# Performance work log

Measured on AMD Instinct MI355X. Metric: run time of the kernel, lower is better.

The kernel has to match this reference:

```python
import jax, jax.numpy as jnp
import numpy as np

EMBED_DIM = 768
NUM_HEADS = 12
HEAD_DIM = EMBED_DIM // NUM_HEADS


def setup_inputs() -> dict:
    key = jax.random.key(0)
    ks = jax.random.split(key, 9)
    B, S, D = 2, 2048, EMBED_DIM
    scale = 1.0 / np.sqrt(D)
    x = jax.random.normal(ks[0], (B, S, D), dtype=jnp.float32)
    Wq = jax.random.normal(ks[1], (D, D), dtype=jnp.float32) * scale
    bq = jax.random.normal(ks[2], (D,), dtype=jnp.float32) * 0.01
    Wk = jax.random.normal(ks[3], (D, D), dtype=jnp.float32) * scale
    bk = jax.random.normal(ks[4], (D,), dtype=jnp.float32) * 0.01
    Wv = jax.random.normal(ks[5], (D, D), dtype=jnp.float32) * scale
    bv = jax.random.normal(ks[6], (D,), dtype=jnp.float32) * 0.01
    Wo = jax.random.normal(ks[7], (D, D), dtype=jnp.float32) * scale
    bo = jax.random.normal(ks[8], (D,), dtype=jnp.float32) * 0.01
    return {"x": x, "Wq": Wq, "bq": bq, "Wk": Wk, "bk": bk,
            "Wv": Wv, "bv": bv, "Wo": Wo, "bo": bo}


def reference(x, Wq, bq, Wk, bk, Wv, bv, Wo, bo):
    B, S, D = x.shape
    H, Dh = NUM_HEADS, HEAD_DIM
    # separate QKV projections (weights stored [in, out] so y = x @ W + b)
    q = (x @ Wq + bq).reshape(B, S, H, Dh)
    k = (x @ Wk + bk).reshape(B, S, H, Dh)
    v = (x @ Wv + bv).reshape(B, S, H, Dh)
    # NOTE: original module applies NO 1/sqrt(head_dim) scaling
    scores = jnp.einsum('bqhd,bkhd->bhqk', q, k)          # [B,H,S,S] materialized
    attn = jax.nn.softmax(scores, axis=-1)
    ctx = jnp.einsum('bhqk,bkhd->bqhd', attn, v)          # [B,S,H,Dh]
    out = ctx.reshape(B, S, D) @ Wo + bo
    return out
```

## Files before the change

kernel.cpp:

```cpp
#include <hip/hip_runtime.h>
#include <hip/hip_bf16.h>


typedef __attribute__((ext_vector_type(8))) short short8;
typedef __attribute__((ext_vector_type(4))) float float4e;
typedef __attribute__((ext_vector_type(16))) float f32x16;

__device__ __forceinline__ ushort f2bf(float f) {
    union { float f; unsigned u; } v; v.f = f;
    unsigned r = v.u + 0x7FFF + ((v.u >> 16) & 1);
    return (ushort)(r >> 16);
}

__device__ __forceinline__ unsigned pk2bf(float a, float b) {
    float2 t; t.x = a; t.y = b;
    __hip_bfloat162 h = __float22bfloat162_rn(t);
    union { __hip_bfloat162 h; unsigned u; } cv; cv.h = h;
    return cv.u;
}

__device__ __forceinline__ void async_cp16(const ushort* g, ushort* l) {
    __builtin_amdgcn_global_load_lds(
        (const __attribute__((address_space(1))) unsigned int*)g,
        (__attribute__((address_space(3))) unsigned int*)l,
        16, 0, 0);
}

__global__ __launch_bounds__(256) void cast_f32_bf16(
    const float* __restrict__ in, ushort* __restrict__ out, int n4)
{
    int i = blockIdx.x * blockDim.x + threadIdx.x;
    if (i < n4) {
        float4 v = *(const float4*)&in[(size_t)i * 4];
        ushort4 o;
        o.x = f2bf(v.x); o.y = f2bf(v.y); o.z = f2bf(v.z); o.w = f2bf(v.w);
        *(ushort4*)&out[(size_t)i * 4] = o;
    }
}

__global__ __launch_bounds__(256) void transpose_cast_w4(
    const float* __restrict__ W0, const float* __restrict__ W1,
    const float* __restrict__ W2, const float* __restrict__ W3,
    ushort* __restrict__ WtBase)
{
    __shared__ float t[64][65];
    const int z = blockIdx.z;
    const float* W = (z == 0) ? W0 : (z == 1) ? W1 : (z == 2) ? W2 : W3;
    ushort* Wt = WtBase + (size_t)z * (768u * 768u);

    const int tid = threadIdx.x;
    const int c  = tid & 63;
    const int rg = tid >> 6;
    const int k0 = blockIdx.y * 64, n0 = blockIdx.x * 64;
    #pragma unroll
    for (int r = 0; r < 16; ++r) {
        const int row = rg * 16 + r;
        t[row][c] = W[(size_t)(k0 + row) * 768 + n0 + c];
    }
    __syncthreads();
    #pragma unroll
    for (int r = 0; r < 16; ++r) {
        const int row = rg * 16 + r;
        Wt[(size_t)(n0 + row) * 768 + k0 + c] = f2bf(t[c][row]);
    }
}

__global__ __launch_bounds__(256) void transpose_v(
    const ushort* __restrict__ Vb, ushort* __restrict__ VT)
{
    __shared__ ushort t[64][72];
    const int tid = threadIdx.x;
    const int b = blockIdx.z, h = blockIdx.y, s0 = blockIdx.x * 64;
    const int lr = tid >> 3;
    const int lc = (tid & 7) * 8;

    #pragma unroll
    for (int half = 0; half < 64; half += 32) {
        const int row = lr + half;
        *(uint4*)&t[row][lc] =
            *(const uint4*)&Vb[(size_t)(b * 2048 + s0 + row) * 768 + h * 64 + lc];
    }
    __syncthreads();
    #pragma unroll
    for (int half = 0; half < 64; half += 32) {
        const int d = lr + half;
        ushort tmp[8];
        #pragma unroll
        for (int i = 0; i < 8; ++i) tmp[i] = t[lc + i][d];
        *(uint4*)&VT[((size_t)(b * 12 + h) * 64 + d) * 2048 + s0 + lc] =
            *(const uint4*)tmp;
    }
}

__global__ __launch_bounds__(256) void gemm_qkv_fused(
    const ushort* __restrict__ A, const ushort* __restrict__ Bt,
    const float* __restrict__ bq, const float* __restrict__ bk,
    const float* __restrict__ bv, ushort* __restrict__ Outbase)
{
    constexpr int K = 768;
    __shared__ ushort As[2][128][32];
    __shared__ ushort Bs[2][128][32];

    const int tid  = threadIdx.x;
    const int w    = tid >> 6;
    const int lane = tid & 63;
    const int l16  = lane & 15;
    const int quad = lane >> 4;
    const int wr   = (w >> 1) * 64;
    const int wc   = (w & 1) * 64;
    const int row0 = blockIdx.y * 128, col0 = blockIdx.x * 128;

    const int r4 = lane >> 2;
    const int c8 = (lane & 3) * 8;

    float4e acc[4][4];
    #pragma unroll
    for (int mi = 0; mi < 4; ++mi)
        #pragma unroll
        for (int ni = 0; ni < 4; ++ni) acc[mi][ni] = (float4e){0.f,0.f,0.f,0.f};

    #pragma unroll
    for (int i = 0; i < 2; ++i) {
        const int rr = w * 32 + i * 16;
        async_cp16(&A [(size_t)(row0 + rr + r4) * K + c8], &As[0][rr][0]);
        async_cp16(&Bt[(size_t)(col0 + rr + r4) * K + c8], &Bs[0][rr][0]);
    }
    __syncthreads();

    for (int k0 = 0; k0 < K; k0 += 32) {
        const int cur = (k0 >> 5) & 1;
        if (k0 + 32 < K) {
            #pragma unroll
            for (int i = 0; i < 2; ++i) {
                const int rr = w * 32 + i * 16;
                async_cp16(&A [(size_t)(row0 + rr + r4) * K + k0 + 32 + c8],
                           &As[cur ^ 1][rr][0]);
                async_cp16(&Bt[(size_t)(col0 + rr + r4) * K + k0 + 32 + c8],
                           &Bs[cur ^ 1][rr][0]);
            }
        }

        short8 af[4], bf[4];
        #pragma unroll
        for (int i = 0; i < 4; ++i) {
            af[i] = *(const short8*)&As[cur][wr + i * 16 + l16][quad * 8];
            bf[i] = *(const short8*)&Bs[cur][wc + i * 16 + l16][quad * 8];
        }
        #pragma unroll
        for (int mi = 0; mi < 4; ++mi)
            #pragma unroll
            for (int ni = 0; ni < 4; ++ni)
                acc[mi][ni] = __builtin_amdgcn_mfma_f32_16x16x32_bf16(
                    af[mi], bf[ni], acc[mi][ni], 0, 0, 0);
        __syncthreads();
    }

    const int seg = (col0 >= 1536) ? 2 : (col0 >= 768 ? 1 : 0);
    const float* bias = (seg == 0) ? bq : (seg == 1) ? bk : bv;
    const int ncol0 = col0 - seg * 768 + wc;
    ushort* outp = Outbase + (size_t)seg * (4096u * 768u);

    #pragma unroll
    for (int ni = 0; ni < 4; ++ni) {
        const int col = ncol0 + ni * 16 + l16;
        const float bs = bias[col];
        #pragma unroll
        for (int mi = 0; mi < 4; ++mi) {
            #pragma unroll
            for (int r = 0; r < 4; ++r) {
                const int row = row0 + wr + mi * 16 + quad * 4 + r;
                outp[(size_t)row * 768 + col] = f2bf(acc[mi][ni][r] + bs);
            }
        }
    }
}

__global__ __launch_bounds__(256) void gemm_wo_128(
    const ushort* __restrict__ A, const ushort* __restrict__ Bt,
    const float* __restrict__ bias, float* __restrict__ Cout)
{
    constexpr int K = 768, N = 768;
    __shared__ ushort As[2][128][32];
    __shared__ ushort Bs[2][128][32];

    const int tid  = threadIdx.x;
    const int w    = tid >> 6;
    const int lane = tid & 63;
    const int l16  = lane & 15;
    const int quad = lane >> 4;
    const int wr   = (w >> 1) * 64;
    const int wc   = (w & 1) * 64;
    const int row0 = blockIdx.y * 128, col0 = blockIdx.x * 128;

    const int r4 = lane >> 2;
    const int c8 = (lane & 3) * 8;

    float4e acc[4][4];
    #pragma unroll
    for (int mi = 0; mi < 4; ++mi)
        #pragma unroll
        for (int ni = 0; ni < 4; ++ni) acc[mi][ni] = (float4e){0.f,0.f,0.f,0.f};

    #pragma unroll
    for (int i = 0; i < 2; ++i) {
        const int rr = w * 32 + i * 16;
        async_cp16(&A [(size_t)(row0 + rr + r4) * K + c8], &As[0][rr][0]);
        async_cp16(&Bt[(size_t)(col0 + rr + r4) * K + c8], &Bs[0][rr][0]);
    }
    __syncthreads();

    for (int k0 = 0; k0 < K; k0 += 32) {
        const int cur = (k0 >> 5) & 1;
        if (k0 + 32 < K) {
            #pragma unroll
            for (int i = 0; i < 2; ++i) {
                const int rr = w * 32 + i * 16;
                async_cp16(&A [(size_t)(row0 + rr + r4) * K + k0 + 32 + c8],
                           &As[cur ^ 1][rr][0]);
                async_cp16(&Bt[(size_t)(col0 + rr + r4) * K + k0 + 32 + c8],
                           &Bs[cur ^ 1][rr][0]);
            }
        }

        short8 af[4], bf[4];
        #pragma unroll
        for (int i = 0; i < 4; ++i) {
            af[i] = *(const short8*)&As[cur][wr + i * 16 + l16][quad * 8];
            bf[i] = *(const short8*)&Bs[cur][wc + i * 16 + l16][quad * 8];
        }
        #pragma unroll
        for (int mi = 0; mi < 4; ++mi)
            #pragma unroll
            for (int ni = 0; ni < 4; ++ni)
                acc[mi][ni] = __builtin_amdgcn_mfma_f32_16x16x32_bf16(
                    af[mi], bf[ni], acc[mi][ni], 0, 0, 0);
        __syncthreads();
    }

    #pragma unroll
    for (int ni = 0; ni < 4; ++ni) {
        const int col = col0 + wc + ni * 16 + l16;
        const float bs = bias[col];
        #pragma unroll
        for (int mi = 0; mi < 4; ++mi) {
            #pragma unroll
            for (int r = 0; r < 4; ++r) {
                const int row = row0 + wr + mi * 16 + quad * 4 + r;
                Cout[(size_t)row * N + col] = acc[mi][ni][r] + bs;
            }
        }
    }
}

__global__ __launch_bounds__(512, 4) void attn_mfma(
    const ushort* __restrict__ Qg, const ushort* __restrict__ Kgl,
    const ushort* __restrict__ VT, ushort* __restrict__ Ctx)
{
    constexpr int S = 2048, D = 768;
    __shared__ union {
        struct {
            ushort Ks [2][128][64];
            ushort Vts[2][64][128];
        } s;
        struct {
            float Osc[6][2048];
            float Msc[6][32];
            float Lsc[6][32];
        } c;
    } U;

    const int tid  = threadIdx.x;
    const int w    = tid >> 6;
    const int qg   = w & 1;
    const int ks   = w >> 1;
    const int lane = tid & 63;
    const int l31  = lane & 31;
    const int hi   = lane >> 5;
    const int b = blockIdx.z, h = blockIdx.y, q0 = blockIdx.x * 64;
    const size_t hc = (size_t)h * 64;

    const size_t qrow = (size_t)(b * S + q0 + qg * 32 + l31) * D + hc + hi * 8;
    short8 yq[4];
    #pragma unroll
    for (int dc = 0; dc < 4; ++dc) yq[dc] = *(const short8*)&Qg[qrow + dc * 16];

    const int sr  = tid >> 3;
    const int kgr = (tid & 7) ^ (sr & 7);
    const ushort* srcK = &Kgl[(size_t)(b * S + sr) * D + hc + kgr * 8];
    const int vr  = tid >> 4;
    const int vgr = (tid & 15) ^ (vr & 7);
    const ushort* srcV = &VT[((size_t)(b * 12 + h) * 64 + vr) * 2048 + vgr * 8];
    ushort* dK0 = &U.s.Ks [0][w * 8][0];
    ushort* dK1 = &U.s.Ks [1][w * 8][0];
    ushort* dV0 = &U.s.Vts[0][w * 4][0];
    ushort* dV1 = &U.s.Vts[1][w * 4][0];

    int okf[4];
    #pragma unroll
    for (int dc = 0; dc < 4; ++dc)
        okf[dc] = (ks * 32 + l31) * 64 + ((dc * 2 + hi) ^ (l31 & 7)) * 8;
    int ovo[2][2][2];
    #pragma unroll
    for (int a = 0; a < 2; ++a)
        #pragma unroll
        for (int m = 0; m < 2; ++m)
            #pragma unroll
            for (int c2 = 0; c2 < 2; ++c2)
                ovo[a][m][c2] = (a * 32 + l31) * 128 +
                    ((ks * 4 + m * 2 + c2) ^ (l31 & 7)) * 8 + hi * 4;

    float m_ = -1e30f, l_ = 0.f;
    f32x16 oa0, oa1;
    #pragma unroll
    for (int i = 0; i < 16; ++i) { oa0[i] = 0.f; oa1[i] = 0.f; }

    async_cp16(srcK,                  dK0);
    async_cp16(srcK + (size_t)64 * D, dK0 + 64 * 64);
    async_cp16(srcV,                  dV0);
    async_cp16(srcV + 32 * 2048,      dV0 + 32 * 128);
    __syncthreads();

    #pragma unroll 2
    for (int t = 0; t < 16; ++t) {
        const int cur = t & 1;
        const ushort* ksb = cur ? &U.s.Ks [1][0][0] : &U.s.Ks [0][0][0];
        const ushort* vsb = cur ? &U.s.Vts[1][0][0] : &U.s.Vts[0][0][0];
        if (t + 1 < 16) {
            const size_t kn = (size_t)(t + 1) * 128;
            ushort* dK = cur ? dK0 : dK1;
            ushort* dV = cur ? dV0 : dV1;
            async_cp16(srcK + kn * D,              dK);
            async_cp16(srcK + (kn + 64) * D,       dK + 64 * 64);
            async_cp16(srcV + kn,                  dV);
            async_cp16(srcV + kn + 32 * 2048,      dV + 32 * 128);
        }

        f32x16 sa;
        #pragma unroll
        for (int i = 0; i < 16; ++i) sa[i] = 0.f;
        __builtin_amdgcn_s_setprio(1);
        #pragma unroll
        for (int dc = 0; dc < 4; ++dc) {
            const short8 xk = *(const short8*)&ksb[okf[dc]];
            sa = __builtin_amdgcn_mfma_f32_32x32x16_bf16(xk, yq[dc], sa, 0, 0, 0);
        }
        __builtin_amdgcn_s_setprio(0);

        float mx = sa[0];
        #pragma unroll
        for (int r = 1; r < 16; ++r) mx = fmaxf(mx, sa[r]);
        mx = fmaxf(mx, __shfl_xor(mx, 32, 64));

        const bool full = !__all(mx - m_ <= 8.f);
        if (full) {
            const float mn = fmaxf(m_, mx);
            const float alpha = __expf(m_ - mn);
            l_ *= alpha;
            m_ = mn;
            #pragma unroll
            for (int i = 0; i < 16; ++i) { oa0[i] *= alpha; oa1[i] *= alpha; }
        }

        float p[16], ps = 0.f;
        #pragma unroll
        for (int r = 0; r < 16; ++r) {
            p[r] = __expf(sa[r] - m_);
            ps += p[r];
        }
        ps += __shfl_xor(ps, 32, 64);
        l_ += ps;

        union { unsigned u[4]; short8 s8; } pa0, pa1;
        pa0.u[0] = pk2bf(p[0],  p[1]);  pa0.u[1] = pk2bf(p[2],  p[3]);
        pa0.u[2] = pk2bf(p[4],  p[5]);  pa0.u[3] = pk2bf(p[6],  p[7]);
        pa1.u[0] = pk2bf(p[8],  p[9]);  pa1.u[1] = pk2bf(p[10], p[11]);
        pa1.u[2] = pk2bf(p[12], p[13]); pa1.u[3] = pk2bf(p[14], p[15]);

        __builtin_amdgcn_s_setprio(1);
        {
            union { uint2 v2[2]; short8 s8; } xv;
            xv.v2[0] = *(const uint2*)&vsb[ovo[0][0][0]];
            xv.v2[1] = *(const uint2*)&vsb[ovo[0][0][1]];
            oa0 = __builtin_amdgcn_mfma_f32_32x32x16_bf16(xv.s8, pa0.s8, oa0, 0, 0, 0);
            xv.v2[0] = *(const uint2*)&vsb[ovo[0][1][0]];
            xv.v2[1] = *(const uint2*)&vsb[ovo[0][1][1]];
            oa0 = __builtin_amdgcn_mfma_f32_32x32x16_bf16(xv.s8, pa1.s8, oa0, 0, 0, 0);
            xv.v2[0] = *(const uint2*)&vsb[ovo[1][0][0]];
            xv.v2[1] = *(const uint2*)&vsb[ovo[1][0][1]];
            oa1 = __builtin_amdgcn_mfma_f32_32x32x16_bf16(xv.s8, pa0.s8, oa1, 0, 0, 0);
            xv.v2[0] = *(const uint2*)&vsb[ovo[1][1][0]];
            xv.v2[1] = *(const uint2*)&vsb[ovo[1][1][1]];
            oa1 = __builtin_amdgcn_mfma_f32_32x32x16_bf16(xv.s8, pa1.s8, oa1, 0, 0, 0);
        }
        __builtin_amdgcn_s_setprio(0);

        __syncthreads();
    }

    if (ks > 0) {
        const int slot = (ks - 1) * 2 + qg;
        float* ob = &U.c.Osc[slot][lane * 32];
        #pragma unroll
        for (int g = 0; g < 4; ++g) {
            float4 v0, v1;
            v0.x = oa0[g * 4 + 0]; v0.y = oa0[g * 4 + 1];
            v0.z = oa0[g * 4 + 2]; v0.w = oa0[g * 4 + 3];
            v1.x = oa1[g * 4 + 0]; v1.y = oa1[g * 4 + 1];
            v1.z = oa1[g * 4 + 2]; v1.w = oa1[g * 4 + 3];
            *(float4*)&ob[(( g     ) ^ (lane & 7)) * 4] = v0;
            *(float4*)&ob[(((g + 4)) ^ (lane & 7)) * 4] = v1;
        }
        if (hi == 0) {
            U.c.Msc[slot][l31] = m_;
            U.c.Lsc[slot][l31] = l_;
        }
    }
    __syncthreads();
    if (ks == 0) {
        const float m1 = U.c.Msc[qg][l31];
        const float m2 = U.c.Msc[2 + qg][l31];
        const float m3 = U.c.Msc[4 + qg][l31];
        const float M  = fmaxf(fmaxf(m_, m1), fmaxf(m2, m3));
        const float a0 = __expf(m_ - M), a1 = __expf(m1 - M),
                    a2 = __expf(m2 - M), a3 = __expf(m3 - M);
        const float l1 = U.c.Lsc[qg][l31];
        const float l2 = U.c.Lsc[2 + qg][l31];
        const float l3 = U.c.Lsc[4 + qg][l31];
        const float inv = 1.0f / (l_ * a0 + l1 * a1 + l2 * a2 + l3 * a3);

        float o[32];
        #pragma unroll
        for (int i = 0; i < 16; ++i) { o[i] = oa0[i] * a0; o[16 + i] = oa1[i] * a0; }
        #pragma unroll
        for (int s = 0; s < 3; ++s) {
            const float as = (s == 0) ? a1 : (s == 1) ? a2 : a3;
            const float* ob = &U.c.Osc[s * 2 + qg][lane * 32];
            #pragma unroll
            for (int gg = 0; gg < 8; ++gg) {
                const float4 v = *(const float4*)&ob[(gg ^ (lane & 7)) * 4];
                o[gg * 4 + 0] += v.x * as;
                o[gg * 4 + 1] += v.y * as;
                o[gg * 4 + 2] += v.z * as;
                o[gg * 4 + 3] += v.w * as;
            }
        }

        const size_t crow = (size_t)(b * S + q0 + qg * 32 + l31) * D + hc;
        #pragma unroll
        for (int a = 0; a < 2; ++a)
            #pragma unroll
            for (int rq = 0; rq < 4; ++rq) {
                const int base = a * 16 + rq * 4;
                uint2 ov;
                ov.x = pk2bf(o[base + 0] * inv, o[base + 1] * inv);
                ov.y = pk2bf(o[base + 2] * inv, o[base + 3] * inv);
                *(uint2*)&Ctx[crow + a * 32 + rq * 8 + hi * 4] = ov;
            }
    }
}

extern "C" void kernel_launch(void* const* d_in, const int* in_sizes, int n_in,
                              void* d_out, int out_size, void* d_ws, size_t ws_size,
                              hipStream_t stream)
{
    const float* x  = (const float*)d_in[0];
    const float* Wq = (const float*)d_in[1];
    const float* bq = (const float*)d_in[2];
    const float* Wk = (const float*)d_in[3];
    const float* bk = (const float*)d_in[4];
    const float* Wv = (const float*)d_in[5];
    const float* bv = (const float*)d_in[6];
    const float* Wo = (const float*)d_in[7];
    const float* bo = (const float*)d_in[8];

    const int M = 4096, D = 768;
    const size_t XE = (size_t)M * D;
    const size_t WE = (size_t)D * D;

    ushort* xb   = (ushort*)d_ws;
    ushort* wtq  = xb   + XE;
    ushort* wto  = wtq  + 3 * WE;
    ushort* qb   = wto  + WE;
    ushort* kb   = qb   + XE;
    ushort* vb   = kb   + XE;
    ushort* ctxb = vb   + XE;
    ushort* vt   = xb;

    cast_f32_bf16<<<(int)(XE / 4 / 256), 256, 0, stream>>>(x, xb, (int)(XE / 4));

    transpose_cast_w4<<<dim3(12, 12, 4), 256, 0, stream>>>(Wq, Wk, Wv, Wo, wtq);

    gemm_qkv_fused<<<dim3(2304 / 128, 4096 / 128), 256, 0, stream>>>(
        xb, wtq, bq, bk, bv, qb);

    transpose_v<<<dim3(32, 12, 2), 256, 0, stream>>>(vb, vt);

    attn_mfma<<<dim3(2048 / 64, 12, 2), 512, 0, stream>>>(qb, kb, vt, ctxb);

    gemm_wo_128<<<dim3(768 / 128, 4096 / 128), 256, 0, stream>>>(
        ctxb, wto, bo, (float*)d_out);
}
```

Before: 182.4 us.

## Load V fragments directly from global in MFMA order, remap blocks by XCD

The V tile is no longer staged through LDS. transpose_v now writes V^T in a permuted column order so that each lane can load its MFMA operand as one 16-byte global load per fragment. This frees LDS, and the launch-bounds occupancy hint is raised from 4 to 6. The attention grid becomes 1D and is remapped so that the blocks on each XCD share the same (batch, head) groups, to improve L2 reuse of K and V. The max reduction is rewritten as a tree. The risk is exposed global-load latency for V inside the loop, since those loads are not prefetched.

After: 257.6 us. 41.3% more time.

```diff
diff --git a/kernel.cpp b/kernel.cpp
--- a/kernel.cpp
+++ b/kernel.cpp
@@ -73,6 +73,8 @@
     const int b = blockIdx.z, h = blockIdx.y, s0 = blockIdx.x * 64;
     const int lr = tid >> 3;
     const int lc = (tid & 7) * 8;
+    const int g  = tid & 7;
+    const int nb = s0 + (g >> 1) * 16 + (g & 1) * 4;
 
     #pragma unroll
     for (int half = 0; half < 64; half += 32) {
@@ -87,8 +89,9 @@
         ushort tmp[8];
         #pragma unroll
         for (int i = 0; i < 8; ++i) tmp[i] = t[lc + i][d];
-        *(uint4*)&VT[((size_t)(b * 12 + h) * 64 + d) * 2048 + s0 + lc] =
-            *(const uint4*)tmp;
+        const size_t row = ((size_t)(b * 12 + h) * 64 + d) * 2048;
+        *(uint2*)&VT[row + nb]     = *(const uint2*)&tmp[0];
+        *(uint2*)&VT[row + nb + 8] = *(const uint2*)&tmp[4];
     }
 }
 
@@ -252,16 +255,13 @@
     }
 }
 
-__global__ __launch_bounds__(512, 4) void attn_mfma(
+__global__ __launch_bounds__(512, 6) void attn_mfma(
     const ushort* __restrict__ Qg, const ushort* __restrict__ Kgl,
     const ushort* __restrict__ VT, ushort* __restrict__ Ctx)
 {
     constexpr int S = 2048, D = 768;
     __shared__ union {
-        struct {
-            ushort Ks [2][128][64];
-            ushort Vts[2][64][128];
-        } s;
+        ushort Ks[2][128][64];
         struct {
             float Osc[6][2048];
             float Msc[6][32];
@@ -276,7 +276,12 @@
     const int lane = tid & 63;
     const int l31  = lane & 31;
     const int hi   = lane >> 5;
-    const int b = blockIdx.z, h = blockIdx.y, q0 = blockIdx.x * 64;
+
+    const int lin = blockIdx.x;
+    const int xcd = lin & 7, sl = lin >> 3;
+    const int grp = xcd * 3 + (sl >> 5);
+    const int q0  = (sl & 31) * 64;
+    const int h   = grp % 12, b = grp / 12;
     const size_t hc = (size_t)h * 64;
 
     const size_t qrow = (size_t)(b * S + q0 + qg * 32 + l31) * D + hc + hi * 8;
@@ -287,27 +292,16 @@
     const int sr  = tid >> 3;
     const int kgr = (tid & 7) ^ (sr & 7);
     const ushort* srcK = &Kgl[(size_t)(b * S + sr) * D + hc + kgr * 8];
-    const int vr  = tid >> 4;
-    const int vgr = (tid & 15) ^ (vr & 7);
-    const ushort* srcV = &VT[((size_t)(b * 12 + h) * 64 + vr) * 2048 + vgr * 8];
-    ushort* dK0 = &U.s.Ks [0][w * 8][0];
-    ushort* dK1 = &U.s.Ks [1][w * 8][0];
-    ushort* dV0 = &U.s.Vts[0][w * 4][0];
-    ushort* dV1 = &U.s.Vts[1][w * 4][0];
+    ushort* dK0 = &U.Ks[0][w * 8][0];
+    ushort* dK1 = &U.Ks[1][w * 8][0];
 
     int okf[4];
     #pragma unroll
     for (int dc = 0; dc < 4; ++dc)
         okf[dc] = (ks * 32 + l31) * 64 + ((dc * 2 + hi) ^ (l31 & 7)) * 8;
-    int ovo[2][2][2];
-    #pragma unroll
-    for (int a = 0; a < 2; ++a)
-        #pragma unroll
-        for (int m = 0; m < 2; ++m)
-            #pragma unroll
-            for (int c2 = 0; c2 < 2; ++c2)
-                ovo[a][m][c2] = (a * 32 + l31) * 128 +
-                    ((ks * 4 + m * 2 + c2) ^ (l31 & 7)) * 8 + hi * 4;
+    const ushort* vp0 = &VT[((size_t)(b * 12 + h) * 64 + l31) * 2048
+                            + ks * 32 + hi * 8];
+    const ushort* vp1 = vp0 + (size_t)32 * 2048;
 
     float m_ = -1e30f, l_ = 0.f;
     f32x16 oa0, oa1;
@@ -316,23 +310,24 @@
 
     async_cp16(srcK,                  dK0);
     async_cp16(srcK + (size_t)64 * D, dK0 + 64 * 64);
-    async_cp16(srcV,                  dV0);
-    async_cp16(srcV + 32 * 2048,      dV0 + 32 * 128);
     __syncthreads();
 
     #pragma unroll 2
     for (int t = 0; t < 16; ++t) {
         const int cur = t & 1;
-        const ushort* ksb = cur ? &U.s.Ks [1][0][0] : &U.s.Ks [0][0][0];
-        const ushort* vsb = cur ? &U.s.Vts[1][0][0] : &U.s.Vts[0][0][0];
+        const ushort* ksb = cur ? &U.Ks[1][0][0] : &U.Ks[0][0][0];
+
+        const int tb = t * 128;
+        const short8 xv00 = *(const short8*)&vp0[tb];
+        const short8 xv01 = *(const short8*)&vp0[tb + 16];
+        const short8 xv10 = *(const short8*)&vp1[tb];
+        const short8 xv11 = *(const short8*)&vp1[tb + 16];
+
         if (t + 1 < 16) {
             const size_t kn = (size_t)(t + 1) * 128;
             ushort* dK = cur ? dK0 : dK1;
-            ushort* dV = cur ? dV0 : dV1;
-            async_cp16(srcK + kn * D,              dK);
-            async_cp16(srcK + (kn + 64) * D,       dK + 64 * 64);
-            async_cp16(srcV + kn,                  dV);
-            async_cp16(srcV + kn + 32 * 2048,      dV + 32 * 128);
+            async_cp16(srcK + kn * D,        dK);
+            async_cp16(srcK + (kn + 64) * D, dK + 64 * 64);
         }
 
         f32x16 sa;
@@ -346,9 +341,12 @@
         }
         __builtin_amdgcn_s_setprio(0);
 
-        float mx = sa[0];
-        #pragma unroll
-        for (int r = 1; r < 16; ++r) mx = fmaxf(mx, sa[r]);
+        float m01 = fmaxf(sa[0], sa[1]),   m23 = fmaxf(sa[2], sa[3]);
+        float m45 = fmaxf(sa[4], sa[5]),   m67 = fmaxf(sa[6], sa[7]);
+        float m89 = fmaxf(sa[8], sa[9]),   mab = fmaxf(sa[10], sa[11]);
+        float mcd = fmaxf(sa[12], sa[13]), mef = fmaxf(sa[14], sa[15]);
+        float mx = fmaxf(fmaxf(fmaxf(m01, m23), fmaxf(m45, m67)),
+                         fmaxf(fmaxf(m89, mab), fmaxf(mcd, mef)));
         mx = fmaxf(mx, __shfl_xor(mx, 32, 64));
 
         const bool full = !__all(mx - m_ <= 8.f);
@@ -377,21 +375,10 @@
         pa1.u[2] = pk2bf(p[12], p[13]); pa1.u[3] = pk2bf(p[14], p[15]);
 
         __builtin_amdgcn_s_setprio(1);
-        {
-            union { uint2 v2[2]; short8 s8; } xv;
-            xv.v2[0] = *(const uint2*)&vsb[ovo[0][0][0]];
-            xv.v2[1] = *(const uint2*)&vsb[ovo[0][0][1]];
-            oa0 = __builtin_amdgcn_mfma_f32_32x32x16_bf16(xv.s8, pa0.s8, oa0, 0, 0, 0);
-            xv.v2[0] = *(const uint2*)&vsb[ovo[0][1][0]];
-            xv.v2[1] = *(const uint2*)&vsb[ovo[0][1][1]];
-            oa0 = __builtin_amdgcn_mfma_f32_32x32x16_bf16(xv.s8, pa1.s8, oa0, 0, 0, 0);
-            xv.v2[0] = *(const uint2*)&vsb[ovo[1][0][0]];
-            xv.v2[1] = *(const uint2*)&vsb[ovo[1][0][1]];
-            oa1 = __builtin_amdgcn_mfma_f32_32x32x16_bf16(xv.s8, pa0.s8, oa1, 0, 0, 0);
-            xv.v2[0] = *(const uint2*)&vsb[ovo[1][1][0]];
-            xv.v2[1] = *(const uint2*)&vsb[ovo[1][1][1]];
-            oa1 = __builtin_amdgcn_mfma_f32_32x32x16_bf16(xv.s8, pa1.s8, oa1, 0, 0, 0);
-        }
+        oa0 = __builtin_amdgcn_mfma_f32_32x32x16_bf16(xv00, pa0.s8, oa0, 0, 0, 0);
+        oa0 = __builtin_amdgcn_mfma_f32_32x32x16_bf16(xv01, pa1.s8, oa0, 0, 0, 0);
+        oa1 = __builtin_amdgcn_mfma_f32_32x32x16_bf16(xv10, pa0.s8, oa1, 0, 0, 0);
+        oa1 = __builtin_amdgcn_mfma_f32_32x32x16_bf16(xv11, pa1.s8, oa1, 0, 0, 0);
         __builtin_amdgcn_s_setprio(0);
 
         __syncthreads();
@@ -495,7 +482,7 @@
 
     transpose_v<<<dim3(32, 12, 2), 256, 0, stream>>>(vb, vt);
 
-    attn_mfma<<<dim3(2048 / 64, 12, 2), 512, 0, stream>>>(qb, kb, vt, ctxb);
+    attn_mfma<<<dim3(768), 512, 0, stream>>>(qb, kb, vt, ctxb);
 
     gemm_wo_128<<<dim3(768 / 128, 4096 / 128), 256, 0, stream>>>(
         ctxb, wto, bo, (float*)d_out);
```
